# Performance work log

Measured on AMD Instinct MI355X. Metric: run time of the kernel, lower is better.

Reference implementation:

```python
import jax, jax.numpy as jnp
import numpy as np

NI = 2048   # num_items
H = 1024    # hidden_size per direction
B = 256     # batch
T = 256     # max seq len


def setup_inputs() -> dict:
    key = jax.random.key(0)
    ks = jax.random.split(key, 12)
    # ragged lengths, contiguous end-padding with 0 (pack_padded_sequence semantics)
    lens = jax.random.randint(ks[0], (B,), 1, T + 1)
    items = jax.random.randint(ks[1], (B, T), 1, NI)      # 0 is padding, valid in [1, NI)
    actions = jax.random.randint(ks[2], (B, T), 1, 3)     # 1=wrong, 2=right
    valid = jnp.arange(T)[None, :] < lens[:, None]
    items = jnp.where(valid, items, 0)
    actions = jnp.where(valid, actions, 0)
    targets = jax.random.randint(ks[3], (B,), 0, 2)
    s = 0.05
    # W_ih stored transposed [2*NI, 4H]: rows [0:NI) for item one-hot, [NI:2NI) for action one-hot
    Wt_f = jax.random.normal(ks[4], (2 * NI, 4 * H), jnp.float32) * s
    Whh_f = jax.random.normal(ks[5], (H, 4 * H), jnp.float32) * s   # stored as h @ Whh
    b_f = jax.random.normal(ks[6], (4 * H,), jnp.float32) * s       # b_ih + b_hh combined
    Wt_b = jax.random.normal(ks[7], (2 * NI, 4 * H), jnp.float32) * s
    Whh_b = jax.random.normal(ks[8], (H, 4 * H), jnp.float32) * s
    b_b = jax.random.normal(ks[9], (4 * H,), jnp.float32) * s
    Wfc = jax.random.normal(ks[10], (2 * H, 2), jnp.float32) * s
    bfc = jax.random.normal(ks[11], (2,), jnp.float32) * s
    return {"items": items, "actions": actions, "targets": targets,
            "Wt_f": Wt_f, "Whh_f": Whh_f, "b_f": b_f,
            "Wt_b": Wt_b, "Whh_b": Whh_b, "b_b": b_b,
            "Wfc": Wfc, "bfc": bfc}


def _lstm_dir(items, actions, lens, Wt, Whh, b, reverse):
    # one_hot(items) @ W_ih.T == gather rows of W_ih.T  (no dense one-hot materialized)
    Bn, Tn = items.shape
    Hn = Whh.shape[0]
    valid = jnp.arange(Tn)[:, None] < lens[None, :]   # [T, B]
    it, ac = items.T, actions.T                        # [T, B]
    if reverse:
        it, ac, valid = it[::-1], ac[::-1], valid[::-1]

    def step(carry, xs):
        h, c = carry
        i_t, a_t, v = xs
        x = Wt[i_t] + Wt[NI + a_t] + b                 # [B, 4H]
        g = x + h @ Whh
        i, f, gg, o = jnp.split(g, 4, axis=-1)         # PyTorch gate order i,f,g,o
        i, f, o = jax.nn.sigmoid(i), jax.nn.sigmoid(f), jax.nn.sigmoid(o)
        c_new = f * c + i * jnp.tanh(gg)
        h_new = o * jnp.tanh(c_new)
        vm = v[:, None]
        # packed semantics: padded steps are not processed -> state frozen
        return (jnp.where(vm, h_new, h), jnp.where(vm, c_new, c)), None

    h0 = jnp.zeros((Bn, Hn), Wt.dtype)
    (h, _), _ = jax.lax.scan(step, (h0, h0), (it, ac, valid))
    return h  # final hidden: last valid step (fwd) / step 0 (bwd)


def reference(items, actions, targets, Wt_f, Whh_f, b_f, Wt_b, Whh_b, b_b, Wfc, bfc):
    lens = (items != 0).sum(1)
    hf = _lstm_dir(items, actions, lens, Wt_f, Whh_f, b_f, False)
    hb = _lstm_dir(items, actions, lens, Wt_b, Whh_b, b_b, True)
    h = jnp.stack([hf, hb])                            # [2, B, H] like torch h
    # F.dropout(p=0.5, training=True), deterministic key for reproducibility
    keep = jax.random.bernoulli(jax.random.key(42), 0.5, h.shape)
    h = jnp.where(keep, h * 2.0, 0.0)
    feat = jnp.concatenate([h[0], h[1]], axis=-1)      # [B, 2H]
    logits = feat @ Wfc + bfc                          # [B, 2]
    logp = jax.nn.log_softmax(logits, axis=-1)
    loss = -jnp.take_along_axis(logp, targets[:, None], axis=1).mean()
    return loss
```

## Files before the change

### kernel.cpp

```cpp
#include <hip/hip_runtime.h>
#include <stdint.h>

typedef uint32_t u32;
typedef __bf16 bf16;
typedef bf16 bf16x8 __attribute__((ext_vector_type(8)));
typedef float f32x4 __attribute__((ext_vector_type(4)));

#define B_ 256
#define T_ 256
#define H_ 1024
#define G_ 4096
#define NI_ 2048

static constexpr size_t OFF_W2T = 0;
static constexpr size_t SZ_W2T  = (size_t)2 * G_ * H_ * 2;
static constexpr size_t OFF_LENS= OFF_W2T + SZ_W2T;
static constexpr size_t OFF_RL  = OFF_LENS + 1024;
static constexpr size_t OFF_BAR = OFF_RL + 1024;
static constexpr size_t SZ_BAR  = 4096;
static constexpr size_t OFF_H   = OFF_BAR + SZ_BAR;
static constexpr size_t SZ_SLOT = (size_t)B_ * H_ * 2;
static constexpr size_t SLOT_U16 = (size_t)B_ * H_;

static constexpr int LDS_BYTES = 131072;

__device__ __forceinline__ float bf2f(uint16_t b){ return __uint_as_float(((u32)b) << 16); }
__device__ __forceinline__ uint16_t f2bf(float f){
  u32 u = __float_as_uint(f);
  return (uint16_t)((u + 0x7fffu + ((u >> 16) & 1u)) >> 16);
}
__device__ __forceinline__ float sigm(float x){ return 1.f / (1.f + __expf(-x)); }
__device__ __forceinline__ float tanh_(float x){ return 1.f - 2.f / (__expf(2.f * x) + 1.f); }

__device__ __forceinline__ void threefry(u32 k0, u32 k1, u32 x0, u32 x1, u32& o0, u32& o1){
  u32 ks2 = k0 ^ k1 ^ 0x1BD11BDAu;
  x0 += k0; x1 += k1;
#define TFR(r) { x0 += x1; x1 = (x1 << r) | (x1 >> (32 - r)); x1 ^= x0; }
  TFR(13) TFR(15) TFR(26) TFR(6)  x0 += k1;  x1 += ks2 + 1u;
  TFR(17) TFR(29) TFR(16) TFR(24) x0 += ks2; x1 += k0 + 2u;
  TFR(13) TFR(15) TFR(26) TFR(6)  x0 += k0;  x1 += k1 + 3u;
  TFR(17) TFR(29) TFR(16) TFR(24) x0 += k1;  x1 += ks2 + 4u;
  TFR(13) TFR(15) TFR(26) TFR(6)  x0 += ks2; x1 += k0 + 5u;
#undef TFR
  o0 = x0; o1 = x1;
}

__device__ __forceinline__ bool keep_mask(u32 idx){
  u32 o0, o1; threefry(0u, 42u, 0u, idx, o0, o1);
  return ((o0 ^ o1) & 0x80000000u) == 0u;
}

__global__ __launch_bounds__(256) void k_prep_w(const float* __restrict__ whh_f,
                                                const float* __restrict__ whh_b,
                                                uint16_t* __restrict__ w2t){
  int bid = blockIdx.x;
  int d  = bid >> 12;
  int r  = bid & 4095;
  int kt = r >> 7;
  int ct = r & 127;
  const float* W = d ? whh_b : whh_f;
  __shared__ float tile[32][33];
  int tid = threadIdx.x;
  int lr = tid >> 5, lc = tid & 31;
#pragma unroll
  for (int i = 0; i < 4; i++)
    tile[lr + i*8][lc] = W[(size_t)(kt*32 + lr + i*8) * G_ + ct*32 + lc];
  __syncthreads();
  int colLocal = tid >> 3, kseg = tid & 7;
  int col = ct*32 + colLocal;
  int strip = col >> 10;
  int hcol  = col & 1023;
  int vcg = (hcol >> 3)*32 + (strip & 1)*16 + (strip >> 1)*8 + (hcol & 7);
  size_t base = ((size_t)d * G_ + vcg) * H_ + kt*32 + kseg*4;
  u32 w0 = (u32)f2bf(tile[kseg*4+0][colLocal]) | ((u32)f2bf(tile[kseg*4+1][colLocal]) << 16);
  u32 w1 = (u32)f2bf(tile[kseg*4+2][colLocal]) | ((u32)f2bf(tile[kseg*4+3][colLocal]) << 16);
  uint2 v; v.x = w0; v.y = w1;
  *(uint2*)(w2t + base) = v;
}

__global__ __launch_bounds__(256) void k_init(uint16_t* __restrict__ hfp,
                                              uint16_t* __restrict__ hbp,
                                              int* __restrict__ lens,
                                              u32* __restrict__ bar,
                                              const int* __restrict__ items){
  int bid = blockIdx.x, tid = threadIdx.x;
  if (bid == 256){
    int cnt = 0;
    for (int t = 0; t < T_; t++) cnt += (items[(size_t)tid * T_ + t] != 0) ? 1 : 0;
    lens[tid] = cnt;
    return;
  }
  size_t g = (size_t)(bid & 127) * 256 + tid;
  uint16_t* hp = (bid < 128) ? hfp : hbp;
  ((uint4*)hp)[g] = make_uint4(0,0,0,0);
  if (bid == 0) ((uint4*)bar)[tid] = make_uint4(0,0,0,0);
}

#define A_LOADC(dst, base, IMM) \
  asm volatile("global_load_dwordx4 %0, %1, off offset:%2 sc0 sc1" \
    : "=v"(dst) : "v"(base), "i"(IMM) : "memory")
#define A_LOADN(dst, base, IMM) \
  asm volatile("global_load_dwordx4 %0, %1, off offset:%2" \
    : "=v"(dst) : "v"(base), "i"(IMM) : "memory")
#define A_WAIT(N, r0, r1) \
  asm volatile("s_waitcnt vmcnt(%2)" : "+v"(r0), "+v"(r1) : "i"(N) : "memory")
#define AISS(j) { if constexpr (CACHED) { \
    A_LOADN(pre0[(j)%10], pA + (size_t)(j)*16384, 0); \
    A_LOADN(pre1[(j)%10], pA + (size_t)(j)*16384, 256); \
  } else { \
    A_LOADC(pre0[(j)%10], pA + (size_t)(j)*16384, 0); \
    A_LOADC(pre1[(j)%10], pA + (size_t)(j)*16384, 256); } }

#define KSTEP(kk) { \
  bf16x8 bb0 = *(const bf16x8*)(smemD +         qoff00 + (((kk)&1)?qd1:qd0) + (((kk)&30)<<6)); \
  bf16x8 bb1 = *(const bf16x8*)(smemD + 32768 + qoff00 + (((kk)&1)?qd1:qd0) + (((kk)&30)<<6)); \
  A_WAIT(((kk)<=21 ? 18 : 62-2*(kk)), pre0[(kk)%10], pre1[(kk)%10]); \
  bf16x8 a0_ = pre0[(kk)%10]; bf16x8 a1_ = pre1[(kk)%10]; \
  accT0[0] = __builtin_amdgcn_mfma_f32_16x16x32_bf16(a0_, bb0, accT0[0], 0,0,0); \
  accT0[1] = __builtin_amdgcn_mfma_f32_16x16x32_bf16(a1_, bb0, accT0[1], 0,0,0); \
  accT1[0] = __builtin_amdgcn_mfma_f32_16x16x32_bf16(a0_, bb1, accT1[0], 0,0,0); \
  accT1[1] = __builtin_amdgcn_mfma_f32_16x16x32_bf16(a1_, bb1, accT1[1], 0,0,0); \
  if ((kk) < 22) { AISS((kk)+10); } }

#define R2(M,a)  M(a) M((a)+1)
#define R4(M,a)  M(a) M((a)+1) M((a)+2) M((a)+3)
#define R10(M,a) R4(M,a) R4(M,(a)+4) R2(M,(a)+8)
#define R16(M,a) R4(M,a) R4(M,(a)+4) R4(M,(a)+8) R4(M,(a)+12)

#define DO_DIR(SMOFF, HINP, HOUTP, XG, XAV, ACV, TT, CREG, HREG, FOFF) \
  { \
    f32x4 accT0[2], accT1[2]; \
    _Pragma("unroll") for (int mi = 0; mi < 2; mi++) \
    _Pragma("unroll") for (int r4 = 0; r4 < 4; r4++){ \
      int i8 = mi*4 + r4; int a_ = ACV[i8]; \
      accT0[mi][r4] = XG[i8][0] + XAV[a_][0]; \
      accT1[mi][r4] = XG[i8][1] + XAV[a_][1]; } \
    asm volatile("s_waitcnt vmcnt(0)" ::: "memory"); \
    __builtin_amdgcn_sched_barrier(0); \
    const char* pA = (const char*)(HINP) + (size_t)(b0 + w*32 + c)*16 + (size_t)lk*4096; \
    const char* smemD = smem + (SMOFF); \
    R10(AISS, 0) \
    R16(KSTEP, 0) R16(KSTEP, 16) \
    __builtin_amdgcn_sched_barrier(0); \
    _Pragma("unroll") for (int mi = 0; mi < 2; mi++) \
    _Pragma("unroll") for (int r4 = 0; r4 < 4; r4++){ \
      int i8 = mi*4 + r4; \
      float u0 = accT0[mi][r4], u1 = accT1[mi][r4]; \
      float v0 = __shfl_xor(u0, 8, 64), v1 = __shfl_xor(u1, 8, 64); \
      float gi = chi ? v0 : u0; \
      float gf = chi ? v1 : u1; \
      float gg = chi ? u0 : v0; \
      float go = chi ? u1 : v1; \
      int row = b0 + w*32 + mi*16 + lk*4 + r4; \
      if ((TT) < len_r[i8]){ \
        float i_ = sigm(gi), f_ = sigm(gf), g_ = tanh_(gg), o_ = sigm(go); \
        float cn = f_ * CREG[i8] + i_ * g_; \
        CREG[i8] = cn; HREG[i8] = f2bf(o_ * tanh_(cn)); } \
      if (!chi){ \
        const uint16_t* addr_ = (HOUTP) + (size_t)n*2048 + (size_t)row*8 + hc8; \
        u32 hv_ = HREG[i8]; \
        asm volatile("global_store_short %0, %1, off sc0 sc1" :: "v"(addr_), "v"(hv_) : "memory"); } \
    } \
    asm volatile("s_waitcnt vmcnt(0)" ::: "memory"); \
  } \
  __syncthreads(); \
  if (tid == 0) __hip_atomic_store(bar + (FOFF) + n, (u32)(s+1), __ATOMIC_RELAXED, __HIP_MEMORY_SCOPE_AGENT);

#define WAITGRP(FOFF, TGT) do { \
  if (tid < 64){ \
    const u32 tgt_ = (u32)(TGT); \
    u32* fp_ = bar + (FOFF); \
    for(;;){ \
      u32 va_ = __hip_atomic_load(fp_ + tid,      __ATOMIC_RELAXED, __HIP_MEMORY_SCOPE_AGENT); \
      u32 vb_ = __hip_atomic_load(fp_ + tid + 64, __ATOMIC_RELAXED, __HIP_MEMORY_SCOPE_AGENT); \
      if (__all(va_ >= tgt_ && vb_ >= tgt_)) break; \
      __builtin_amdgcn_s_sleep(1); \
    } \
  } \
  __syncthreads(); \
} while(0)

template <bool CACHED>
__global__ __launch_bounds__(256, 1) void k_persist(
    const int* __restrict__ items, const int* __restrict__ actions,
    const float* __restrict__ wt_f, const float* __restrict__ wt_b,
    const float* __restrict__ bias_f, const float* __restrict__ bias_b,
    const uint16_t* __restrict__ w2t, uint16_t* __restrict__ hf, uint16_t* __restrict__ hb,
    const int* __restrict__ lens, u32* __restrict__ bar, int rmask)
{
  extern __shared__ char smem[];
  const int bid = blockIdx.x;
  const int m = (bid >> 2) & 1;
  const int n = (bid >> 3) * 4 + (bid & 3);
  const int tid = threadIdx.x;
  const int b0 = m * 128;

#pragma unroll
  for (int dd = 0; dd < 2; dd++){
    const char* wsrc = (const char*)(w2t + ((size_t)dd * G_ + n*32) * H_);
#pragma unroll
    for (int i = 0; i < 16; i++){
      int u = i*256 + tid;
      int row = u >> 7, seg = u & 127;
      int sb = seg * 16;
      uint4 v = *(const uint4*)(wsrc + row*2048 + sb);
      *(uint4*)(smem + dd*65536 + row*2048 + (sb ^ ((row & 7) << 4))) = v;
    }
  }

  const int w   = tid >> 6;
  const int l   = tid & 63;
  const int c   = l & 15;
  const int lk  = l >> 4;
  const int hc8 = c & 7;
  const int chi = (c >> 3) & 1;
  const int gcol0 = (chi ? 2 : 0)*1024 + n*8 + hc8;
  const int gcol1 = (chi ? 3 : 1)*1024 + n*8 + hc8;

  float xavf[3][2], xavb[3][2];
#pragma unroll
  for (int a = 0; a < 3; a++){
    xavf[a][0] = wt_f[(size_t)(NI_ + a) * G_ + gcol0] + bias_f[gcol0];
    xavf[a][1] = wt_f[(size_t)(NI_ + a) * G_ + gcol1] + bias_f[gcol1];
    xavb[a][0] = wt_b[(size_t)(NI_ + a) * G_ + gcol0] + bias_b[gcol0];
    xavb[a][1] = wt_b[(size_t)(NI_ + a) * G_ + gcol1] + bias_b[gcol1];
  }

  int len_r[8];
#pragma unroll
  for (int i = 0; i < 8; i++)
    len_r[i] = lens[b0 + w*32 + (i>>2)*16 + lk*4 + (i&3)];

  int itf[8], acf[8], itb[8], acb[8];
  float xgf[8][2], xgb[8][2];
#pragma unroll
  for (int i = 0; i < 8; i++){
    int row = b0 + w*32 + (i>>2)*16 + lk*4 + (i&3);
    itf[i] = items[(size_t)row * T_ + 0];        acf[i] = actions[(size_t)row * T_ + 0];
    itb[i] = items[(size_t)row * T_ + (T_-1)];   acb[i] = actions[(size_t)row * T_ + (T_-1)];
  }
#pragma unroll
  for (int i = 0; i < 8; i++){
    xgf[i][0] = wt_f[(size_t)itf[i] * G_ + gcol0]; xgf[i][1] = wt_f[(size_t)itf[i] * G_ + gcol1];
    xgb[i][0] = wt_b[(size_t)itb[i] * G_ + gcol0]; xgb[i][1] = wt_b[(size_t)itb[i] * G_ + gcol1];
  }

  const int key  = (c & 7) << 4;
  const int kbit = (c >> 2) & 1;
  const u32 qoff00 = (u32)(c*2048 + ((lk*16) ^ (key & 48)));
  const u32 qd0 = (u32)((kbit) << 6);
  const u32 qd1 = (u32)((1 ^ kbit) << 6);

  float crf[8], crb[8]; uint16_t hrf[8], hrb[8];
#pragma unroll
  for (int i = 0; i < 8; i++){ crf[i] = 0.f; crb[i] = 0.f; hrf[i] = 0; hrb[i] = 0; }

  __syncthreads();

  bf16x8 pre0[10], pre1[10];

  for (int s = 0; s < T_; s++){
    if (CACHED && s != 0 && ((s & rmask) == 0))
      __builtin_amdgcn_fence(__ATOMIC_ACQUIRE, "agent");

    const int tf = s, tb = T_-1-s;
    const uint16_t* hfin  = hf + (size_t)(s & rmask) * SLOT_U16;
    uint16_t*       hfout = hf + (size_t)((s+1) & rmask) * SLOT_U16;
    const uint16_t* hbin  = hb + (size_t)(s & rmask) * SLOT_U16;
    uint16_t*       hbout = hb + (size_t)((s+1) & rmask) * SLOT_U16;

    DO_DIR(0, hfin, hfout, xgf, xavf, acf, tf, crf, hrf, m*128)
    if (s) { WAITGRP(256 + m*128, (u32)s); }
    DO_DIR(65536, hbin, hbout, xgb, xavb, acb, tb, crb, hrb, 256 + m*128)
    if (s == T_-1) break;

    {
      int tf2 = s + 1, tb2 = T_ - 2 - s;
#pragma unroll
      for (int i = 0; i < 8; i++){
        int row = b0 + w*32 + (i>>2)*16 + lk*4 + (i&3);
        itf[i] = items[(size_t)row * T_ + tf2]; acf[i] = actions[(size_t)row * T_ + tf2];
        itb[i] = items[(size_t)row * T_ + tb2]; acb[i] = actions[(size_t)row * T_ + tb2];
      }
#pragma unroll
      for (int i = 0; i < 8; i++){
        xgf[i][0] = wt_f[(size_t)itf[i] * G_ + gcol0]; xgf[i][1] = wt_f[(size_t)itf[i] * G_ + gcol1];
        xgb[i][0] = wt_b[(size_t)itb[i] * G_ + gcol0]; xgb[i][1] = wt_b[(size_t)itb[i] * G_ + gcol1];
      }
    }
    WAITGRP(m*128, (u32)(s+1));
  }
}

__global__ __launch_bounds__(256) void k_fc(const uint16_t* __restrict__ hfq,
    const uint16_t* __restrict__ hbq,
    const float* __restrict__ wfc, const float* __restrict__ bfc,
    const int* __restrict__ targets, float* __restrict__ rowloss){
  int b = blockIdx.x, tid = threadIdx.x;
  float a0 = 0.f, a1 = 0.f;
  for (int jj = tid; jj < 2*H_; jj += 256){
    int d = jj >> 10, j = jj & 1023;
    const uint16_t* hp = d ? hbq : hfq;
    float h = bf2f(hp[(size_t)(j >> 3) * 2048 + (size_t)b * 8 + (j & 7)]);
    u32 idx = (u32)(d * (B_ * H_) + b * H_ + j);
    float feat = keep_mask(idx) ? (2.f * h) : 0.f;
    a0 += feat * wfc[jj*2 + 0];
    a1 += feat * wfc[jj*2 + 1];
  }
#pragma unroll
  for (int off = 32; off > 0; off >>= 1){
    a0 += __shfl_down(a0, off, 64);
    a1 += __shfl_down(a1, off, 64);
  }
  __shared__ float r0[4], r1[4];
  if ((tid & 63) == 0){ r0[tid >> 6] = a0; r1[tid >> 6] = a1; }
  __syncthreads();
  if (tid == 0){
    float l0 = r0[0]+r0[1]+r0[2]+r0[3] + bfc[0];
    float l1 = r1[0]+r1[1]+r1[2]+r1[3] + bfc[1];
    float mx = fmaxf(l0, l1);
    float lse = mx + logf(__expf(l0 - mx) + __expf(l1 - mx));
    rowloss[b] = lse - (targets[b] ? l1 : l0);
  }
}

__global__ __launch_bounds__(256) void k_loss(const float* __restrict__ rowloss, float* __restrict__ out){
  int tid = threadIdx.x;
  float v = rowloss[tid];
#pragma unroll
  for (int off = 32; off > 0; off >>= 1) v += __shfl_down(v, off, 64);
  __shared__ float r[4];
  if ((tid & 63) == 0) r[tid >> 6] = v;
  __syncthreads();
  if (tid == 0) out[0] = (r[0] + r[1] + r[2] + r[3]) * (1.f / B_);
}

extern "C" void kernel_launch(void* const* d_in, const int* in_sizes, int n_in,
                              void* d_out, int out_size, void* d_ws, size_t ws_size,
                              hipStream_t stream){
  (void)in_sizes; (void)n_in; (void)out_size;
  const int*   items   = (const int*)  d_in[0];
  const int*   actions = (const int*)  d_in[1];
  const int*   targets = (const int*)  d_in[2];
  const float* wt_f    = (const float*)d_in[3];
  const float* whh_f   = (const float*)d_in[4];
  const float* b_f     = (const float*)d_in[5];
  const float* wt_b    = (const float*)d_in[6];
  const float* whh_b   = (const float*)d_in[7];
  const float* b_b     = (const float*)d_in[8];
  const float* wfc     = (const float*)d_in[9];
  const float* bfc     = (const float*)d_in[10];

  char* ws = (char*)d_ws;
  uint16_t* w2t   = (uint16_t*)(ws + OFF_W2T);
  int*      lens  = (int*)     (ws + OFF_LENS);
  float*    rlbuf = (float*)   (ws + OFF_RL);
  u32*      bar   = (u32*)     (ws + OFF_BAR);
  uint16_t* hf    = (uint16_t*)(ws + OFF_H);

  int R = 0;
  if      (ws_size >= OFF_H + 32u * SZ_SLOT) R = 16;
  else if (ws_size >= OFF_H + 16u * SZ_SLOT) R = 8;
  else if (ws_size >= OFF_H +  8u * SZ_SLOT) R = 4;
  int rmask = R ? (R - 1) : 1;
  int Reff  = R ? R : 2;
  uint16_t* hb = hf + (size_t)Reff * SLOT_U16;

  hipFuncSetAttribute((const void*)k_persist<true>,
                      hipFuncAttributeMaxDynamicSharedMemorySize, LDS_BYTES);
  hipFuncSetAttribute((const void*)k_persist<false>,
                      hipFuncAttributeMaxDynamicSharedMemorySize, LDS_BYTES);

  hipLaunchKernelGGL(k_prep_w, dim3(8192), dim3(256), 0, stream, whh_f, whh_b, w2t);
  hipLaunchKernelGGL(k_init,   dim3(257),  dim3(256), 0, stream, hf, hb, lens, bar, items);

  void* args[] = { (void*)&items, (void*)&actions, (void*)&wt_f, (void*)&wt_b,
                   (void*)&b_f, (void*)&b_b, (void*)&w2t, (void*)&hf, (void*)&hb,
                   (void*)&lens, (void*)&bar, (void*)&rmask };
  if (R)
    hipLaunchCooperativeKernel((const void*)k_persist<true>, dim3(256), dim3(256),
                               args, LDS_BYTES, stream);
  else
    hipLaunchCooperativeKernel((const void*)k_persist<false>, dim3(256), dim3(256),
                               args, LDS_BYTES, stream);

  hipLaunchKernelGGL(k_fc,   dim3(256), dim3(256), 0, stream, hf, hb, wfc, bfc, targets, rlbuf);
  hipLaunchKernelGGL(k_loss, dim3(1),   dim3(256), 0, stream, rlbuf, (float*)d_out);
}
```

Measured before the change: 3.642 ms.

## Split LSTM directions across separate persistent blocks, two blocks per CU

The persistent kernel now launches 512 blocks. Each block handles one direction, holding only that direction's Whh slice in LDS (64KB plus a staging area), so two blocks can reside per CU. Forward and backward recurrences run independently with per-direction flag barriers instead of interleaving both directions in one block. Hidden-state outputs are staged through LDS and written as dwordx2 stores instead of scattered short stores. The cost is more blocks contending for each CU's compute and memory, and the change relies on all 512 blocks being co-resident for the cooperative launch.

```diff
diff --git a/kernel.cpp b/kernel.cpp
--- a/kernel.cpp
+++ b/kernel.cpp
@@ -5,6 +5,7 @@
 typedef __bf16 bf16;
 typedef bf16 bf16x8 __attribute__((ext_vector_type(8)));
 typedef float f32x4 __attribute__((ext_vector_type(4)));
+typedef uint32_t u32x2 __attribute__((ext_vector_type(2)));
 
 #define B_ 256
 #define T_ 256
@@ -22,7 +23,8 @@
 static constexpr size_t SZ_SLOT = (size_t)B_ * H_ * 2;
 static constexpr size_t SLOT_U16 = (size_t)B_ * H_;
 
-static constexpr int LDS_BYTES = 131072;
+static constexpr int STG_OFF   = 65536;
+static constexpr int LDS_BYTES = 65536 + 2048;
 
 __device__ __forceinline__ float bf2f(uint16_t b){ return __uint_as_float(((u32)b) << 16); }
 __device__ __forceinline__ uint16_t f2bf(float f){
@@ -112,8 +114,8 @@
     A_LOADC(pre1[(j)%10], pA + (size_t)(j)*16384, 256); } }
 
 #define KSTEP(kk) { \
-  bf16x8 bb0 = *(const bf16x8*)(smemD +         qoff00 + (((kk)&1)?qd1:qd0) + (((kk)&30)<<6)); \
-  bf16x8 bb1 = *(const bf16x8*)(smemD + 32768 + qoff00 + (((kk)&1)?qd1:qd0) + (((kk)&30)<<6)); \
+  bf16x8 bb0 = *(const bf16x8*)(smem +         qoff00 + (((kk)&1)?qd1:qd0) + (((kk)&30)<<6)); \
+  bf16x8 bb1 = *(const bf16x8*)(smem + 32768 + qoff00 + (((kk)&1)?qd1:qd0) + (((kk)&30)<<6)); \
   A_WAIT(((kk)<=21 ? 18 : 62-2*(kk)), pre0[(kk)%10], pre1[(kk)%10]); \
   bf16x8 a0_ = pre0[(kk)%10]; bf16x8 a1_ = pre1[(kk)%10]; \
   accT0[0] = __builtin_amdgcn_mfma_f32_16x16x32_bf16(a0_, bb0, accT0[0], 0,0,0); \
@@ -127,61 +129,8 @@
 #define R10(M,a) R4(M,a) R4(M,(a)+4) R2(M,(a)+8)
 #define R16(M,a) R4(M,a) R4(M,(a)+4) R4(M,(a)+8) R4(M,(a)+12)
 
-#define DO_DIR(SMOFF, HINP, HOUTP, XG, XAV, ACV, TT, CREG, HREG, FOFF) \
-  { \
-    f32x4 accT0[2], accT1[2]; \
-    _Pragma("unroll") for (int mi = 0; mi < 2; mi++) \
-    _Pragma("unroll") for (int r4 = 0; r4 < 4; r4++){ \
-      int i8 = mi*4 + r4; int a_ = ACV[i8]; \
-      accT0[mi][r4] = XG[i8][0] + XAV[a_][0]; \
-      accT1[mi][r4] = XG[i8][1] + XAV[a_][1]; } \
-    asm volatile("s_waitcnt vmcnt(0)" ::: "memory"); \
-    __builtin_amdgcn_sched_barrier(0); \
-    const char* pA = (const char*)(HINP) + (size_t)(b0 + w*32 + c)*16 + (size_t)lk*4096; \
-    const char* smemD = smem + (SMOFF); \
-    R10(AISS, 0) \
-    R16(KSTEP, 0) R16(KSTEP, 16) \
-    __builtin_amdgcn_sched_barrier(0); \
-    _Pragma("unroll") for (int mi = 0; mi < 2; mi++) \
-    _Pragma("unroll") for (int r4 = 0; r4 < 4; r4++){ \
-      int i8 = mi*4 + r4; \
-      float u0 = accT0[mi][r4], u1 = accT1[mi][r4]; \
-      float v0 = __shfl_xor(u0, 8, 64), v1 = __shfl_xor(u1, 8, 64); \
-      float gi = chi ? v0 : u0; \
-      float gf = chi ? v1 : u1; \
-      float gg = chi ? u0 : v0; \
-      float go = chi ? u1 : v1; \
-      int row = b0 + w*32 + mi*16 + lk*4 + r4; \
-      if ((TT) < len_r[i8]){ \
-        float i_ = sigm(gi), f_ = sigm(gf), g_ = tanh_(gg), o_ = sigm(go); \
-        float cn = f_ * CREG[i8] + i_ * g_; \
-        CREG[i8] = cn; HREG[i8] = f2bf(o_ * tanh_(cn)); } \
-      if (!chi){ \
-        const uint16_t* addr_ = (HOUTP) + (size_t)n*2048 + (size_t)row*8 + hc8; \
-        u32 hv_ = HREG[i8]; \
-        asm volatile("global_store_short %0, %1, off sc0 sc1" :: "v"(addr_), "v"(hv_) : "memory"); } \
-    } \
-    asm volatile("s_waitcnt vmcnt(0)" ::: "memory"); \
-  } \
-  __syncthreads(); \
-  if (tid == 0) __hip_atomic_store(bar + (FOFF) + n, (u32)(s+1), __ATOMIC_RELAXED, __HIP_MEMORY_SCOPE_AGENT);
-
-#define WAITGRP(FOFF, TGT) do { \
-  if (tid < 64){ \
-    const u32 tgt_ = (u32)(TGT); \
-    u32* fp_ = bar + (FOFF); \
-    for(;;){ \
-      u32 va_ = __hip_atomic_load(fp_ + tid,      __ATOMIC_RELAXED, __HIP_MEMORY_SCOPE_AGENT); \
-      u32 vb_ = __hip_atomic_load(fp_ + tid + 64, __ATOMIC_RELAXED, __HIP_MEMORY_SCOPE_AGENT); \
-      if (__all(va_ >= tgt_ && vb_ >= tgt_)) break; \
-      __builtin_amdgcn_s_sleep(1); \
-    } \
-  } \
-  __syncthreads(); \
-} while(0)
-
 template <bool CACHED>
-__global__ __launch_bounds__(256, 1) void k_persist(
+__global__ __launch_bounds__(256, 2) void k_persist(
     const int* __restrict__ items, const int* __restrict__ actions,
     const float* __restrict__ wt_f, const float* __restrict__ wt_b,
     const float* __restrict__ bias_f, const float* __restrict__ bias_b,
@@ -190,21 +139,25 @@
 {
   extern __shared__ char smem[];
   const int bid = blockIdx.x;
-  const int m = (bid >> 2) & 1;
-  const int n = (bid >> 3) * 4 + (bid & 3);
+  const int d = bid & 1;
+  const int m = (bid >> 1) & 1;
+  const int n = bid >> 2;
   const int tid = threadIdx.x;
   const int b0 = m * 128;
-
-#pragma unroll
-  for (int dd = 0; dd < 2; dd++){
-    const char* wsrc = (const char*)(w2t + ((size_t)dd * G_ + n*32) * H_);
+  const float* wt   = d ? wt_b : wt_f;
+  const float* bias = d ? bias_b : bias_f;
+  uint16_t* hbase = d ? hb : hf;
+  u32* flg = bar + ((u32)(d*2 + m) << 7);
+
+  {
+    const char* wsrc = (const char*)(w2t + ((size_t)d * G_ + n*32) * H_);
 #pragma unroll
     for (int i = 0; i < 16; i++){
       int u = i*256 + tid;
       int row = u >> 7, seg = u & 127;
       int sb = seg * 16;
       uint4 v = *(const uint4*)(wsrc + row*2048 + sb);
-      *(uint4*)(smem + dd*65536 + row*2048 + (sb ^ ((row & 7) << 4))) = v;
+      *(uint4*)(smem + row*2048 + (sb ^ ((row & 7) << 4))) = v;
     }
   }
 
@@ -217,13 +170,11 @@
   const int gcol0 = (chi ? 2 : 0)*1024 + n*8 + hc8;
   const int gcol1 = (chi ? 3 : 1)*1024 + n*8 + hc8;
 
-  float xavf[3][2], xavb[3][2];
+  float xav[3][2];
 #pragma unroll
   for (int a = 0; a < 3; a++){
-    xavf[a][0] = wt_f[(size_t)(NI_ + a) * G_ + gcol0] + bias_f[gcol0];
-    xavf[a][1] = wt_f[(size_t)(NI_ + a) * G_ + gcol1] + bias_f[gcol1];
-    xavb[a][0] = wt_b[(size_t)(NI_ + a) * G_ + gcol0] + bias_b[gcol0];
-    xavb[a][1] = wt_b[(size_t)(NI_ + a) * G_ + gcol1] + bias_b[gcol1];
+    xav[a][0] = wt[(size_t)(NI_ + a) * G_ + gcol0] + bias[gcol0];
+    xav[a][1] = wt[(size_t)(NI_ + a) * G_ + gcol1] + bias[gcol1];
   }
 
   int len_r[8];
@@ -231,18 +182,18 @@
   for (int i = 0; i < 8; i++)
     len_r[i] = lens[b0 + w*32 + (i>>2)*16 + lk*4 + (i&3)];
 
-  int itf[8], acf[8], itb[8], acb[8];
-  float xgf[8][2], xgb[8][2];
-#pragma unroll
-  for (int i = 0; i < 8; i++){
-    int row = b0 + w*32 + (i>>2)*16 + lk*4 + (i&3);
-    itf[i] = items[(size_t)row * T_ + 0];        acf[i] = actions[(size_t)row * T_ + 0];
-    itb[i] = items[(size_t)row * T_ + (T_-1)];   acb[i] = actions[(size_t)row * T_ + (T_-1)];
-  }
-#pragma unroll
-  for (int i = 0; i < 8; i++){
-    xgf[i][0] = wt_f[(size_t)itf[i] * G_ + gcol0]; xgf[i][1] = wt_f[(size_t)itf[i] * G_ + gcol1];
-    xgb[i][0] = wt_b[(size_t)itb[i] * G_ + gcol0]; xgb[i][1] = wt_b[(size_t)itb[i] * G_ + gcol1];
+  int ac_c[8];
+  float xg[8][2];
+  {
+    const int t0 = d ? (T_-1) : 0;
+#pragma unroll
+    for (int i = 0; i < 8; i++){
+      int row = b0 + w*32 + (i>>2)*16 + lk*4 + (i&3);
+      int it = items[(size_t)row * T_ + t0];
+      ac_c[i] = actions[(size_t)row * T_ + t0];
+      xg[i][0] = wt[(size_t)it * G_ + gcol0];
+      xg[i][1] = wt[(size_t)it * G_ + gcol1];
+    }
   }
 
   const int key  = (c & 7) << 4;
@@ -251,44 +202,105 @@
   const u32 qd0 = (u32)((kbit) << 6);
   const u32 qd1 = (u32)((1 ^ kbit) << 6);
 
-  float crf[8], crb[8]; uint16_t hrf[8], hrb[8];
-#pragma unroll
-  for (int i = 0; i < 8; i++){ crf[i] = 0.f; crb[i] = 0.f; hrf[i] = 0; hrb[i] = 0; }
+  float c_reg[8]; uint16_t h_reg[8];
+#pragma unroll
+  for (int i = 0; i < 8; i++){ c_reg[i] = 0.f; h_reg[i] = 0; }
 
   __syncthreads();
 
   bf16x8 pre0[10], pre1[10];
 
   for (int s = 0; s < T_; s++){
-    if (CACHED && s != 0 && ((s & rmask) == 0))
-      __builtin_amdgcn_fence(__ATOMIC_ACQUIRE, "agent");
-
-    const int tf = s, tb = T_-1-s;
-    const uint16_t* hfin  = hf + (size_t)(s & rmask) * SLOT_U16;
-    uint16_t*       hfout = hf + (size_t)((s+1) & rmask) * SLOT_U16;
-    const uint16_t* hbin  = hb + (size_t)(s & rmask) * SLOT_U16;
-    uint16_t*       hbout = hb + (size_t)((s+1) & rmask) * SLOT_U16;
-
-    DO_DIR(0, hfin, hfout, xgf, xavf, acf, tf, crf, hrf, m*128)
-    if (s) { WAITGRP(256 + m*128, (u32)s); }
-    DO_DIR(65536, hbin, hbout, xgb, xavb, acb, tb, crb, hrb, 256 + m*128)
+    const int t = d ? (T_-1-s) : s;
+
+    f32x4 accT0[2], accT1[2];
+#pragma unroll
+    for (int mi = 0; mi < 2; mi++)
+#pragma unroll
+      for (int r4 = 0; r4 < 4; r4++){
+        int i8 = mi*4 + r4; int a_ = ac_c[i8];
+        accT0[mi][r4] = xg[i8][0] + xav[a_][0];
+        accT1[mi][r4] = xg[i8][1] + xav[a_][1];
+      }
+
+    if (s){
+      if (tid < 64){
+        const u32 tgt = (u32)s;
+        for(;;){
+          u32 va = __hip_atomic_load(flg + tid,      __ATOMIC_RELAXED, __HIP_MEMORY_SCOPE_AGENT);
+          u32 vb = __hip_atomic_load(flg + 64 + tid, __ATOMIC_RELAXED, __HIP_MEMORY_SCOPE_AGENT);
+          if (__all(va >= tgt && vb >= tgt)) break;
+          __builtin_amdgcn_s_sleep(1);
+        }
+      }
+      __syncthreads();
+      if (CACHED && ((s & rmask) == 0))
+        __builtin_amdgcn_fence(__ATOMIC_ACQUIRE, "agent");
+    }
+
+    asm volatile("s_waitcnt vmcnt(0)" ::: "memory");
+    __builtin_amdgcn_sched_barrier(0);
+
+    const uint16_t* hin  = hbase + (size_t)(s & rmask)     * SLOT_U16;
+    uint16_t*       hout = hbase + (size_t)((s+1) & rmask) * SLOT_U16;
+    const char* pA = (const char*)hin + (size_t)(b0 + w*32 + c)*16 + (size_t)lk*4096;
+
+    R10(AISS, 0)
+    R16(KSTEP, 0) R16(KSTEP, 16)
+    __builtin_amdgcn_sched_barrier(0);
+
+#pragma unroll
+    for (int mi = 0; mi < 2; mi++)
+#pragma unroll
+      for (int r4 = 0; r4 < 4; r4++){
+        int i8 = mi*4 + r4;
+        float u0 = accT0[mi][r4], u1 = accT1[mi][r4];
+        float v0 = __shfl_xor(u0, 8, 64), v1 = __shfl_xor(u1, 8, 64);
+        float gi = chi ? v0 : u0;
+        float gf = chi ? v1 : u1;
+        float gg = chi ? u0 : v0;
+        float go = chi ? u1 : v1;
+        if (t < len_r[i8]){
+          float i_ = sigm(gi), f_ = sigm(gf), g_ = tanh_(gg), o_ = sigm(go);
+          float cn = f_ * c_reg[i8] + i_ * g_;
+          c_reg[i8] = cn;
+          h_reg[i8] = f2bf(o_ * tanh_(cn));
+        }
+      }
+
+    {
+      uint16_t* stg = (uint16_t*)(smem + STG_OFF + w*512);
+      if (!chi){
+#pragma unroll
+        for (int i8 = 0; i8 < 8; i8++){
+          int rl = (i8 >> 2)*16 + lk*4 + (i8 & 3);
+          stg[rl*8 + hc8] = h_reg[i8];
+        }
+      }
+      u32x2 pk = *(const u32x2*)((const char*)smem + STG_OFF + w*512 + l*8);
+      const char* addr = (const char*)hout + (size_t)n*4096 + (size_t)(b0 + w*32)*16 + (size_t)l*8;
+      asm volatile("global_store_dwordx2 %0, %1, off sc0 sc1" :: "v"(addr), "v"(pk) : "memory");
+    }
+    asm volatile("s_waitcnt vmcnt(0)" ::: "memory");
+    __syncthreads();
     if (s == T_-1) break;
 
+    if (tid == 0)
+      __hip_atomic_store(flg + n, (u32)(s+1), __ATOMIC_RELEASE, __HIP_MEMORY_SCOPE_AGENT);
+
     {
-      int tf2 = s + 1, tb2 = T_ - 2 - s;
+      int t2 = d ? (T_-2-s) : (s+1);
+      if (t2 < 0) t2 = 0;
+      if (t2 > T_-1) t2 = T_-1;
 #pragma unroll
       for (int i = 0; i < 8; i++){
         int row = b0 + w*32 + (i>>2)*16 + lk*4 + (i&3);
-        itf[i] = items[(size_t)row * T_ + tf2]; acf[i] = actions[(size_t)row * T_ + tf2];
-        itb[i] = items[(size_t)row * T_ + tb2]; acb[i] = actions[(size_t)row * T_ + tb2];
-      }
-#pragma unroll
-      for (int i = 0; i < 8; i++){
-        xgf[i][0] = wt_f[(size_t)itf[i] * G_ + gcol0]; xgf[i][1] = wt_f[(size_t)itf[i] * G_ + gcol1];
-        xgb[i][0] = wt_b[(size_t)itb[i] * G_ + gcol0]; xgb[i][1] = wt_b[(size_t)itb[i] * G_ + gcol1];
+        int it = items[(size_t)row * T_ + t2];
+        ac_c[i] = actions[(size_t)row * T_ + t2];
+        xg[i][0] = wt[(size_t)it * G_ + gcol0];
+        xg[i][1] = wt[(size_t)it * G_ + gcol1];
       }
     }
-    WAITGRP(m*128, (u32)(s+1));
   }
 }
 
@@ -378,10 +390,10 @@
                    (void*)&b_f, (void*)&b_b, (void*)&w2t, (void*)&hf, (void*)&hb,
                    (void*)&lens, (void*)&bar, (void*)&rmask };
   if (R)
-    hipLaunchCooperativeKernel((const void*)k_persist<true>, dim3(256), dim3(256),
+    hipLaunchCooperativeKernel((const void*)k_persist<true>, dim3(512), dim3(256),
                                args, LDS_BYTES, stream);
   else
-    hipLaunchCooperativeKernel((const void*)k_persist<false>, dim3(256), dim3(256),
+    hipLaunchCooperativeKernel((const void*)k_persist<false>, dim3(512), dim3(256),
                                args, LDS_BYTES, stream);
 
   hipLaunchKernelGGL(k_fc,   dim3(256), dim3(256), 0, stream, hf, hb, wfc, bfc, targets, rlbuf);
```

New measurement: 5.555 ms. 1.53x slower.
